# Kernel optimization log

Hardware: AMD Instinct MI355X
Metric: run time of the kernel (lower is better)

The kernel has to match this reference:

```python
import jax, jax.numpy as jnp
import numpy as np

CH_IN, CH_OUT, CH, NLAYERS = 40, 9, 64, 10
CH_CLOSE = 2 * CH
KSZ = 9  # stencil hard-coded to 9 in init_weights
H = 0.1


def conv1(X, Ker):
    # F.conv1d(X, Ker, padding=(k-1)//2); Ker: (Cout, Cin, k)
    pad = (Ker.shape[-1] - 1) // 2
    return jax.lax.conv_general_dilated(X, Ker, (1,), [(pad, pad)],
                                        dimension_numbers=('NCH', 'OIH', 'NCH'))


def conv1T(X, Ker):
    # F.conv_transpose1d(X, Ker, padding=(k-1)//2) with stride 1 ==
    # conv1d with swapped in/out channels and flipped taps, padding k-1-(k-1)//2
    k = Ker.shape[-1]
    pad = k - 1 - (k - 1) // 2
    Kt = jnp.flip(jnp.swapaxes(Ker, 0, 1), -1)
    return jax.lax.conv_general_dilated(X, Kt, (1,), [(pad, pad)],
                                        dimension_numbers=('NCH', 'OIH', 'NCH'))


def mean_masked(X, mask, axis, keepdims=False):
    return jnp.sum(X * mask, axis=axis, keepdims=keepdims) / jnp.sum(mask, axis=axis, keepdims=keepdims)


def tr2dist(Y):
    # pairwise distances of columns of Y (B,C,N) -> (B,N,N), per Pfold tr2DistSmall
    k = Y.shape[1]
    Z = Y - jnp.mean(Y, axis=2, keepdims=True)
    n2 = jnp.sum(Z * Z, axis=1)  # (B,N)
    D = n2[:, :, None] + n2[:, None, :] - 2.0 * jnp.einsum('bcn,bcm->bnm', Z, Z)
    D = 3.0 * D / k
    Dr = jnp.maximum(D, 0.0)
    safe = jnp.where(Dr > 0, Dr, 1.0)  # grad-safe sqrt
    return jnp.where(Dr > 0, jnp.sqrt(safe), 0.0)


def get_graph_lap(X, mask, sigma):
    # X: (B,C,N), mask: (B,1,N)
    mm = jnp.einsum('bci,bcj->bij', mask, mask)  # (B,N,N) pair mask
    msum = jnp.sum(mask, axis=2, keepdims=True)
    Xc = X - (jnp.sum(X * mask, axis=2, keepdims=True) / msum) * mask
    Xc = Xc / jnp.sqrt(jnp.sum(Xc * Xc, axis=2, keepdims=True) / msum + 1e-4)
    N = X.shape[2]
    pos = 0.5 * jnp.linspace(0.0, 1.0, N)[None, None, :] * mask  # (B,1,N)
    Xa = jnp.concatenate([Xc, pos], axis=1)
    W = tr2dist(Xa) * mm
    W = jnp.exp(-W / sigma * 10.0) * mm
    Wsum = jnp.sum(W, axis=1)  # (B,N)
    D = Wsum[:, :, None] * jnp.eye(N, dtype=W.dtype)  # diag(Wsum)
    L = D - W
    return 0.5 * (L + jnp.swapaxes(L, 1, 2)), W


def double_sym(Z, Wi, Bi, L, mask):
    A0 = conv1(Z + Bi[0], Wi[0]) * mask
    A0 = (A0 - mean_masked(A0, mask, 2, True)) * mask
    A0 = A0 / jnp.sqrt(jnp.sum(A0 * A0, axis=1, keepdims=True) + 1e-3)
    A1 = (conv1(Z + Bi[1], Wi[1]) @ L) * mask
    A1 = (A1 - mean_masked(A1, mask, 2, True)) * mask
    A1 = A1 / jnp.sqrt(jnp.sum(A1 * A1, axis=1, keepdims=True) + 1e-3)
    A0 = jax.nn.relu(A0)
    A1 = jax.nn.relu(A1)
    A0 = conv1T(A0, Wi[0]) * mask
    A1 = (conv1T(A1, Wi[1]) @ L) * mask
    return A0 + A1


def hypernet_forward(Z, mask, Kopen, Kclose, W, Bias):
    mask = mask[:, None, :]  # (B,1,N)
    Z = jnp.einsum('ci,bin->bcn', Kopen, Z) * mask
    L, _ = get_graph_lap(Z, mask, 10.0)
    for i in range(W.shape[0]):
        if i % 10 == 0:
            L, _ = get_graph_lap(Z, mask, 10.0)
        Z = Z - H * double_sym(Z, W[i], Bias[i], L, mask)
    Z = jnp.einsum('oc,bcn->bon', Kclose, Z) * mask
    dists = jnp.stack([tr2dist(Z[:, 3 * i:3 * i + 3, :]) for i in range(Z.shape[1] // 3)], axis=1)
    return dists, Z  # dists: (B, chan_out//3, N, N)


def setup_inputs() -> dict:
    key = jax.random.key(0)
    ks = jax.random.split(key, 5)
    B, N = 8, 1024
    Z = jax.random.normal(ks[0], (B, CH_IN, N), dtype=jnp.float32)
    mask = jnp.ones((B, N), dtype=jnp.float32)
    so = float(CH) / CH_IN
    Kopen = jax.random.uniform(ks[1], (CH, CH_IN), minval=-so, maxval=so, dtype=jnp.float32)
    sc = float(CH_OUT) / CH
    Kclose = jax.random.uniform(ks[2], (CH_OUT, CH), minval=-sc, maxval=sc, dtype=jnp.float32)
    W = jax.random.uniform(ks[3], (NLAYERS, 2, CH_CLOSE, CH, KSZ), minval=-0.1, maxval=0.1, dtype=jnp.float32)
    Bias = jax.random.uniform(ks[4], (NLAYERS, 2, CH, 1), dtype=jnp.float32) * 0.001
    return {"Z": Z, "mask": mask, "Kopen": Kopen, "Kclose": Kclose, "W": W, "Bias": Bias}


def reference(Z, mask, Kopen, Kclose, W, Bias):
    return hypernet_forward(Z, mask, Kopen, Kclose, W, Bias)
```

## Files before the change

kernel.cpp:

```cpp
#include <hip/hip_runtime.h>
#include <cstddef>

#define BB 8
#define NN 1024
#define CIN 40
#define CH 64
#define CC 128
#define COUT 9
#define KS 9
#define NL 10
#define HSTEP 0.1f
#define SKC 2
#define SKH 4

typedef __attribute__((ext_vector_type(8))) short bf16x8;
typedef __attribute__((ext_vector_type(4))) float f32x4;

__device__ __forceinline__ unsigned short f2bf(float f) {
    union { float f; unsigned u; } v;
    v.f = f;
    unsigned u = v.u;
    u += 0x7FFFu + ((u >> 16) & 1u);
    return (unsigned short)(u >> 16);
}
__device__ __forceinline__ float bf2f(unsigned short h) {
    union { unsigned u; float f; } v;
    v.u = ((unsigned)h) << 16;
    return v.f;
}

__device__ __forceinline__ size_t pk_addr(int lb, int row, int col, int R, int KDv) {
    int chunk = ((lb * (R / 32) + (row >> 5)) * (KDv / 32) + (col >> 5)) * 2 + ((row >> 4) & 1);
    int lane = ((col >> 3) & 3) * 16 + (row & 15);
    return ((size_t)chunk * 64 + lane) * 8 + (col & 7);
}

__device__ __forceinline__ float blockSum(float v, float* red) {
    int tid = threadIdx.x;
    red[tid] = v;
    __syncthreads();
    for (int s = 128; s > 0; s >>= 1) {
        if (tid < s) red[tid] += red[tid + s];
        __syncthreads();
    }
    float r = red[0];
    __syncthreads();
    return r;
}

__global__ __launch_bounds__(256) void k_zero(float* __restrict__ p, int n) {
    int i = blockIdx.x * 256 + threadIdx.x;
    if (i < n) p[i] = 0.f;
}

__global__ __launch_bounds__(256) void k_prep_wbf(const float* __restrict__ Win,
                                                  unsigned short* __restrict__ PKc_h,
                                                  unsigned short* __restrict__ PKc_l,
                                                  unsigned short* __restrict__ PKt_h,
                                                  unsigned short* __restrict__ PKt_l) {
    int idx = blockIdx.x * 256 + threadIdx.x;
    const int total = NL * 2 * CC * CH * KS;
    if (idx >= total) return;
    int k = idx % KS;
    int t = idx / KS;
    int i = t % CH;  t /= CH;
    int o = t % CC;  t /= CC;
    int lb = t;
    float v = Win[idx];
    unsigned short h = f2bf(v);
    unsigned short l = f2bf(v - bf2f(h));
    size_t ac = pk_addr(lb, o, k * 64 + i, CC, 576);
    size_t at = pk_addr(lb, i, (8 - k) * 128 + o, CH, 1152);
    PKc_h[ac] = h;
    PKc_l[ac] = l;
    PKt_h[at] = h;
    PKt_l[at] = l;
}

__global__ __launch_bounds__(256) void k_prep_bks(const float* __restrict__ Win,
                                                  const float* __restrict__ Bias,
                                                  float* __restrict__ bks) {
    int idx = blockIdx.x * 256 + threadIdx.x;
    const int total = NL * 2 * CC * KS;
    if (idx >= total) return;
    int k = idx % KS;
    int t = idx / KS;
    int o = t % CC;
    int lb = t / CC;
    float s = 0.f;
    for (int i = 0; i < CH; ++i)
        s += Win[(((size_t)lb * CC + o) * CH + i) * KS + k] * Bias[lb * CH + i];
    bks[idx] = s;
}

__global__ __launch_bounds__(256) void k_open(const float* __restrict__ Zin,
                                              const float* __restrict__ mask,
                                              const float* __restrict__ Kop,
                                              float* __restrict__ Zcur) {
    int n = blockIdx.x * 256 + threadIdx.x;
    int c = blockIdx.y, b = blockIdx.z;
    float acc = 0.f;
    for (int i = 0; i < CIN; ++i)
        acc += Kop[c * CIN + i] * Zin[((size_t)b * CIN + i) * NN + n];
    Zcur[((size_t)b * CH + c) * NN + n] = acc * mask[b * NN + n];
}

__global__ __launch_bounds__(256) void k_za(const float* __restrict__ Zcur,
                                            const float* __restrict__ mask,
                                            float* __restrict__ Za) {
    __shared__ float red[256];
    int c = blockIdx.x;
    int b = blockIdx.y;
    int tid = threadIdx.x;
    const float* m = mask + b * NN;
    float x[4], mv[4];
    if (c < CH) {
        const float* src = Zcur + ((size_t)b * CH + c) * NN;
#pragma unroll
        for (int j = 0; j < 4; ++j) { int n = tid * 4 + j; x[j] = src[n]; mv[j] = m[n]; }
    } else {
#pragma unroll
        for (int j = 0; j < 4; ++j) { int n = tid * 4 + j; mv[j] = m[n]; x[j] = 0.5f * ((float)n / 1023.f) * mv[j]; }
    }
    float sm = 0.f, sxm = 0.f;
#pragma unroll
    for (int j = 0; j < 4; ++j) { sm += mv[j]; sxm += x[j] * mv[j]; }
    float msum = blockSum(sm, red);
    float xm = blockSum(sxm, red);
    if (c < CH) {
        float mean = xm / msum;
        float ss = 0.f;
#pragma unroll
        for (int j = 0; j < 4; ++j) { x[j] -= mean * mv[j]; ss += x[j] * x[j]; }
        ss = blockSum(ss, red);
        float sc = rsqrtf(ss / msum + 1e-4f);
#pragma unroll
        for (int j = 0; j < 4; ++j) x[j] *= sc;
    }
    float ps = 0.f;
#pragma unroll
    for (int j = 0; j < 4; ++j) ps += x[j];
    float pm = blockSum(ps, red) / (float)NN;
    float* dst = Za + ((size_t)b * 65 + c) * NN;
#pragma unroll
    for (int j = 0; j < 4; ++j) dst[tid * 4 + j] = x[j] - pm;
}

__global__ __launch_bounds__(256) void k_n2g(const float* __restrict__ Za, float* __restrict__ n2g) {
    int n = blockIdx.x * 256 + threadIdx.x;
    int b = blockIdx.y;
    float s = 0.f;
    for (int c = 0; c < 65; ++c) { float v = Za[((size_t)b * 65 + c) * NN + n]; s += v * v; }
    n2g[b * NN + n] = s;
}

__global__ __launch_bounds__(256) void k_gramW(const float* __restrict__ Za,
                                               const float* __restrict__ n2g,
                                               const float* __restrict__ mask,
                                               unsigned short* __restrict__ Wpk,
                                               float* __restrict__ Wsum) {
    __shared__ float As[65][64];
    __shared__ float Bs2[65][64];
    __shared__ unsigned short wt[64][72];
    __shared__ float csred[16][64];
    int i0 = blockIdx.x * 64, j0 = blockIdx.y * 64, b = blockIdx.z;
    int tid = threadIdx.x;
    for (int e = tid; e < 65 * 64; e += 256) {
        int c = e >> 6, t = e & 63;
        const float* src = Za + ((size_t)b * 65 + c) * NN;
        As[c][t] = src[i0 + t];
        Bs2[c][t] = src[j0 + t];
    }
    __syncthreads();
    int tx = tid & 15, ty = tid >> 4;
    float acc[4][4] = {};
    for (int c = 0; c < 65; ++c) {
        float a[4];
#pragma unroll
        for (int q = 0; q < 4; ++q) a[q] = As[c][ty * 4 + q];
        float bv[4];
        *reinterpret_cast<float4*>(bv) = *reinterpret_cast<const float4*>(&Bs2[c][tx * 4]);
#pragma unroll
        for (int q = 0; q < 4; ++q)
#pragma unroll
            for (int r = 0; r < 4; ++r) acc[q][r] += a[q] * bv[r];
    }
    const float* m = mask + b * NN;
    float csacc[4] = {0.f, 0.f, 0.f, 0.f};
    for (int q = 0; q < 4; ++q) {
        int i = i0 + ty * 4 + q;
        float n2i = n2g[b * NN + i], mi = m[i];
#pragma unroll
        for (int r = 0; r < 4; ++r) {
            int j = j0 + tx * 4 + r;
            float D = n2i + n2g[b * NN + j] - 2.f * acc[q][r];
            D *= (3.f / 65.f);
            D = fmaxf(D, 0.f);
            float dist = (D > 0.f) ? sqrtf(D) : 0.f;
            float mmv = mi * m[j];
            float res = expf(-dist * mmv) * mmv;
            wt[ty * 4 + q][tx * 4 + r] = f2bf(res);
            csacc[r] += res;
        }
    }
#pragma unroll
    for (int r = 0; r < 4; ++r) csred[ty][tx * 4 + r] = csacc[r];
    __syncthreads();
    for (int s = 8; s > 0; s >>= 1) {
        if (ty < s) {
#pragma unroll
            for (int r = 0; r < 4; ++r) csred[ty][tx * 4 + r] += csred[ty + s][tx * 4 + r];
        }
        __syncthreads();
    }
    if (ty == 0) {
#pragma unroll
        for (int r = 0; r < 4; ++r)
            atomicAdd(&Wsum[b * NN + j0 + tx * 4 + r], csred[0][tx * 4 + r]);
    }
    for (int e = tid; e < 512; e += 256) {
        int li = e >> 3, ljb = (e & 7) * 8;
        int row = i0 + li, col = j0 + ljb;
        int chunk = ((b * 32 + (row >> 5)) * 32 + (col >> 5)) * 2 + ((row >> 4) & 1);
        int lane2 = ((col >> 3) & 3) * 16 + (row & 15);
        unsigned short* dp = Wpk + ((size_t)chunk * 64 + lane2) * 8;
        *reinterpret_cast<ushort4*>(dp) = *reinterpret_cast<ushort4*>(&wt[li][ljb]);
        *reinterpret_cast<ushort4*>(dp + 4) = *reinterpret_cast<ushort4*>(&wt[li][ljb + 4]);
    }
}

__global__ __launch_bounds__(256) void k_conv1_mfma(const float* __restrict__ Zcur,
                                                    const unsigned short* __restrict__ Wh,
                                                    const unsigned short* __restrict__ Wl,
                                                    const float* __restrict__ bksl,
                                                    const float* __restrict__ mask,
                                                    float* __restrict__ C0,
                                                    float* __restrict__ C1,
                                                    unsigned short* __restrict__ C1pk) {
    __shared__ __align__(16) unsigned short xh[80][64];
    __shared__ __align__(16) unsigned short xl[80][64];
    int n0 = blockIdx.x * 64;
    int y = blockIdx.y;
    int b = blockIdx.z;
    int br = y >> 1, half = y & 1;
    int tid = threadIdx.x;
    const float* Xb = Zcur + (size_t)b * CH * NN;

    for (int e = tid; e < 64 * 20; e += 256) {
        int i = e / 20, t = e - i * 20;
        int gn = n0 + t * 4 - 4;
        float4 v = make_float4(0.f, 0.f, 0.f, 0.f);
        if (gn >= 0 && gn + 3 < NN) v = *reinterpret_cast<const float4*>(&Xb[(size_t)i * NN + gn]);
        float vv[4] = {v.x, v.y, v.z, v.w};
#pragma unroll
        for (int j = 0; j < 4; ++j) {
            int row = t * 4 + j;
            int col = i ^ ((row & 7) << 3);
            unsigned short h = f2bf(vv[j]);
            xh[row][col] = h;
            xl[row][col] = f2bf(vv[j] - bf2f(h));
        }
    }
    __syncthreads();

    int wid = tid >> 6, lane = tid & 63;
    int wo = (wid >> 1) * 32, wn = (wid & 1) * 32;
    int r = lane & 15, g = lane >> 4;
    int r32 = half * 2 + (wid >> 1);
    size_t brOff = (size_t)br * (CC / 32) * (576 / 32) * 1024;

    f32x4 acc[2][2] = {};
#pragma unroll 3
    for (int q = 0; q < 18; ++q) {
        int k = q >> 1, s = q & 1;
        size_t widx = brOff + ((size_t)(r32 * 18 + q)) * 1024 + lane * 8;
        bf16x8 ah[2], al[2];
        ah[0] = *reinterpret_cast<const bf16x8*>(&Wh[widx]);
        ah[1] = *reinterpret_cast<const bf16x8*>(&Wh[widx + 512]);
        al[0] = *reinterpret_cast<const bf16x8*>(&Wl[widx]);
        al[1] = *reinterpret_cast<const bf16x8*>(&Wl[widx + 512]);
        bf16x8 bh[2], bl[2];
#pragma unroll
        for (int fn = 0; fn < 2; ++fn) {
            int row = wn + fn * 16 + r + k;
            int chs = (s * 32 + g * 8) ^ ((row & 7) << 3);
            bh[fn] = *reinterpret_cast<const bf16x8*>(&xh[row][chs]);
            bl[fn] = *reinterpret_cast<const bf16x8*>(&xl[row][chs]);
        }
#pragma unroll
        for (int fc = 0; fc < 2; ++fc)
#pragma unroll
            for (int fn = 0; fn < 2; ++fn) {
                acc[fc][fn] = __builtin_amdgcn_mfma_f32_16x16x32_bf16(ah[fc], bh[fn], acc[fc][fn], 0, 0, 0);
                acc[fc][fn] = __builtin_amdgcn_mfma_f32_16x16x32_bf16(al[fc], bh[fn], acc[fc][fn], 0, 0, 0);
                acc[fc][fn] = __builtin_amdgcn_mfma_f32_16x16x32_bf16(ah[fc], bl[fn], acc[fc][fn], 0, 0, 0);
            }
    }

    const float* mkB = mask + b * NN;
    float* Outp = (br ? C1 : C0) + ((size_t)b * CC + half * 64) * NN;
    const float* bo_base = bksl + (br * CC + half * 64) * KS;
#pragma unroll
    for (int fc = 0; fc < 2; ++fc) {
#pragma unroll
        for (int fn = 0; fn < 2; ++fn) {
            int n = n0 + wn + fn * 16 + r;
#pragma unroll
            for (int rr = 0; rr < 4; ++rr) {
                int oo = wo + fc * 16 + 4 * g + rr;
                float v = acc[fc][fn][rr];
                const float* bo = bo_base + oo * KS;
                float bias = 0.f;
#pragma unroll
                for (int k = 0; k < KS; ++k) {
                    int nn2 = n + k - 4;
                    if (nn2 >= 0 && nn2 < NN) bias += bo[k];
                }
                v += bias;
                if (br == 0) v *= mkB[n];
                Outp[(size_t)oo * NN + n] = v;
                if (br == 1) {
                    int cg = half * 64 + oo;
                    int chunk = ((b * 4 + (cg >> 5)) * 32 + (n >> 5)) * 2 + ((cg >> 4) & 1);
                    int lane2 = ((n >> 3) & 3) * 16 + (cg & 15);
                    C1pk[((size_t)chunk * 64 + lane2) * 8 + (n & 7)] = f2bf(v);
                }
            }
        }
    }
}

__global__ __launch_bounds__(256) void k_convT_mfma(const float* __restrict__ C0,
                                                    const float* __restrict__ A1,
                                                    const unsigned short* __restrict__ Wh,
                                                    const unsigned short* __restrict__ Wl,
                                                    const float* __restrict__ mask,
                                                    const float* __restrict__ meanA,
                                                    const float* __restrict__ invA,
                                                    float* __restrict__ T0,
                                                    float* __restrict__ T1p,
                                                    unsigned short* __restrict__ T1pk) {
    __shared__ __align__(16) unsigned short xh[48][128];
    __shared__ __align__(16) unsigned short xl[48][128];
    __shared__ float red2[2][32][33];
    int n0 = blockIdx.x * 32;
    int br = blockIdx.y;
    int b = blockIdx.z;
    int tid = threadIdx.x;
    const float* Xb = (br ? A1 : C0) + (size_t)b * CC * NN;
    const float* meB = meanA + ((size_t)br * BB + b) * CC;
    const float* ivB = invA + ((size_t)br * BB + b) * NN;
    const float* mkB = mask + b * NN;

    for (int e = tid; e < 128 * 12; e += 256) {
        int i = e / 12, t = e - i * 12;
        int gn = n0 + t * 4 - 4;
        float4 v = make_float4(0.f, 0.f, 0.f, 0.f);
        if (gn >= 0 && gn + 3 < NN) {
            v = *reinterpret_cast<const float4*>(&Xb[(size_t)i * NN + gn]);
            float me = meB[i];
            float4 iv = *reinterpret_cast<const float4*>(&ivB[gn]);
            float4 mk = *reinterpret_cast<const float4*>(&mkB[gn]);
            v.x = fmaxf((v.x - me) * mk.x * iv.x, 0.f);
            v.y = fmaxf((v.y - me) * mk.y * iv.y, 0.f);
            v.z = fmaxf((v.z - me) * mk.z * iv.z, 0.f);
            v.w = fmaxf((v.w - me) * mk.w * iv.w, 0.f);
        }
        float vv[4] = {v.x, v.y, v.z, v.w};
#pragma unroll
        for (int j = 0; j < 4; ++j) {
            int row = t * 4 + j;
            int col = i ^ ((row & 7) << 3);
            unsigned short h = f2bf(vv[j]);
            xh[row][col] = h;
            xl[row][col] = f2bf(vv[j] - bf2f(h));
        }
    }
    __syncthreads();

    int wid = tid >> 6, lane = tid & 63;
    int i32 = wid & 1, kh = wid >> 1;
    int r = lane & 15, g = lane >> 4;
    size_t brW = (size_t)br * (CH / 32) * (1152 / 32) * 1024;

    f32x4 acc[2][2] = {};
#pragma unroll 3
    for (int t = 0; t < 18; ++t) {
        int k = t >> 1, s = kh * 2 + (t & 1);
        int q32 = k * 4 + s;
        size_t widx = brW + ((size_t)(i32 * 36 + q32)) * 1024 + lane * 8;
        bf16x8 ah[2], al[2];
        ah[0] = *reinterpret_cast<const bf16x8*>(&Wh[widx]);
        ah[1] = *reinterpret_cast<const bf16x8*>(&Wh[widx + 512]);
        al[0] = *reinterpret_cast<const bf16x8*>(&Wl[widx]);
        al[1] = *reinterpret_cast<const bf16x8*>(&Wl[widx + 512]);
        bf16x8 bh[2], bl[2];
#pragma unroll
        for (int fn = 0; fn < 2; ++fn) {
            int row = fn * 16 + r + k;
            int chs = (s * 32 + g * 8) ^ ((row & 7) << 3);
            bh[fn] = *reinterpret_cast<const bf16x8*>(&xh[row][chs]);
            bl[fn] = *reinterpret_cast<const bf16x8*>(&xl[row][chs]);
        }
#pragma unroll
        for (int fc = 0; fc < 2; ++fc)
#pragma unroll
            for (int fn = 0; fn < 2; ++fn) {
                acc[fc][fn] = __builtin_amdgcn_mfma_f32_16x16x32_bf16(ah[fc], bh[fn], acc[fc][fn], 0, 0, 0);
                acc[fc][fn] = __builtin_amdgcn_mfma_f32_16x16x32_bf16(al[fc], bh[fn], acc[fc][fn], 0, 0, 0);
                acc[fc][fn] = __builtin_amdgcn_mfma_f32_16x16x32_bf16(ah[fc], bl[fn], acc[fc][fn], 0, 0, 0);
            }
    }

    if (kh == 1) {
#pragma unroll
        for (int fc = 0; fc < 2; ++fc)
#pragma unroll
            for (int fn = 0; fn < 2; ++fn)
#pragma unroll
                for (int rr = 0; rr < 4; ++rr)
                    red2[i32][fc * 16 + 4 * g + rr][fn * 16 + r] = acc[fc][fn][rr];
    }
    __syncthreads();
    if (kh == 0) {
        float* Outp = (br ? T1p : T0) + (size_t)b * CH * NN;
#pragma unroll
        for (int fc = 0; fc < 2; ++fc)
#pragma unroll
            for (int fn = 0; fn < 2; ++fn) {
                int n = n0 + fn * 16 + r;
#pragma unroll
                for (int rr = 0; rr < 4; ++rr) {
                    int irow = fc * 16 + 4 * g + rr;
                    float v = acc[fc][fn][rr] + red2[i32][irow][fn * 16 + r];
                    Outp[(size_t)(i32 * 32 + irow) * NN + n] = v;
                    if (br == 1) {
                        int cg = i32 * 32 + irow;
                        int chunk = ((b * 2 + (cg >> 5)) * 32 + (n >> 5)) * 2 + ((cg >> 4) & 1);
                        int lane2 = ((n >> 3) & 3) * 16 + (cg & 15);
                        T1pk[((size_t)chunk * 64 + lane2) * 8 + (n & 7)] = f2bf(v);
                    }
                }
            }
    }
}

template <int SKN>
__global__ __launch_bounds__(256) void k_matL_mfma(const unsigned short* __restrict__ Xpk,
                                                   const unsigned short* __restrict__ Wpk,
                                                   float* __restrict__ Part, int rows) {
    int cb = rows >> 6;
    int sk = blockIdx.y;
    int b = blockIdx.z / cb;
    int c0 = (blockIdx.z % cb) * 64;
    int tid = threadIdx.x;
    int wid = tid >> 6, lane = tid & 63;
    int wc = (wid >> 1) * 32;
    int r = lane & 15, g = lane >> 4;
    int rowsT = rows >> 5;
    int ct = (c0 >> 5) + (wid >> 1);
    int nt32 = blockIdx.x * 2 + (wid & 1);
    const unsigned short* Xb = Xpk + ((size_t)(b * rowsT + ct)) * 32768 + (size_t)lane * 8;
    const unsigned short* Wb = Wpk + ((size_t)(b * 32 + nt32)) * 32768 + (size_t)lane * 8;

    f32x4 acc[2][2] = {};
    int ms_beg = sk * (32 / SKN);
#pragma unroll 4
    for (int ms = ms_beg; ms < ms_beg + 32 / SKN; ++ms) {
        bf16x8 a0 = *reinterpret_cast<const bf16x8*>(&Xb[(size_t)ms * 1024]);
        bf16x8 a1 = *reinterpret_cast<const bf16x8*>(&Xb[(size_t)ms * 1024 + 512]);
        bf16x8 w0 = *reinterpret_cast<const bf16x8*>(&Wb[(size_t)ms * 1024]);
        bf16x8 w1 = *reinterpret_cast<const bf16x8*>(&Wb[(size_t)ms * 1024 + 512]);
        acc[0][0] = __builtin_amdgcn_mfma_f32_16x16x32_bf16(a0, w0, acc[0][0], 0, 0, 0);
        acc[0][1] = __builtin_amdgcn_mfma_f32_16x16x32_bf16(a0, w1, acc[0][1], 0, 0, 0);
        acc[1][0] = __builtin_amdgcn_mfma_f32_16x16x32_bf16(a1, w0, acc[1][0], 0, 0, 0);
        acc[1][1] = __builtin_amdgcn_mfma_f32_16x16x32_bf16(a1, w1, acc[1][1], 0, 0, 0);
    }
    int n0 = blockIdx.x * 64;
    int wn = (wid & 1) * 32;
#pragma unroll
    for (int fc = 0; fc < 2; ++fc)
#pragma unroll
        for (int fn = 0; fn < 2; ++fn) {
            int ncol = n0 + wn + fn * 16 + r;
#pragma unroll
            for (int rr = 0; rr < 4; ++rr) {
                int crow = c0 + wc + fc * 16 + 4 * g + rr;
                Part[(((size_t)b * SKN + sk) * rows + crow) * NN + ncol] = acc[fc][fn][rr];
            }
        }
}

template <int SKN, int MODE>
__global__ __launch_bounds__(256) void k_matL_fin(const float* __restrict__ X,
                                                  const float* __restrict__ Part,
                                                  const float* __restrict__ Wsum,
                                                  const float* __restrict__ mask,
                                                  const float* __restrict__ T0,
                                                  float* __restrict__ Out,
                                                  float* __restrict__ meanA, int rows) {
    __shared__ float red[256];
    int c = blockIdx.x, b = blockIdx.y;
    int n = threadIdx.x * 4;
    float4 s = make_float4(0.f, 0.f, 0.f, 0.f);
#pragma unroll
    for (int sk = 0; sk < SKN; ++sk) {
        float4 p = *reinterpret_cast<const float4*>(
            &Part[(((size_t)b * SKN + sk) * rows + c) * NN + n]);
        s.x += p.x; s.y += p.y; s.z += p.z; s.w += p.w;
    }
    float4 xv = *reinterpret_cast<const float4*>(&X[((size_t)b * rows + c) * NN + n]);
    float4 wv = *reinterpret_cast<const float4*>(&Wsum[b * NN + n]);
    float4 mv = *reinterpret_cast<const float4*>(&mask[b * NN + n]);
    float y0 = xv.x * wv.x - s.x, y1 = xv.y * wv.y - s.y;
    float y2 = xv.z * wv.z - s.z, y3 = xv.w * wv.w - s.w;
    if (MODE == 0) {
        float4 res = make_float4(y0 * mv.x, y1 * mv.y, y2 * mv.z, y3 * mv.w);
        *reinterpret_cast<float4*>(&Out[((size_t)b * rows + c) * NN + n]) = res;
        float rs = res.x * mv.x + res.y * mv.y + res.z * mv.z + res.w * mv.w;
        float ms = mv.x + mv.y + mv.z + mv.w;
        rs = blockSum(rs, red);
        ms = blockSum(ms, red);
        if (threadIdx.x == 0) meanA[((size_t)BB + b) * CC + c] = rs / ms;
    } else {
        float4 t0 = *reinterpret_cast<const float4*>(&T0[((size_t)b * rows + c) * NN + n]);
        float4 o = *reinterpret_cast<const float4*>(&Out[((size_t)b * rows + c) * NN + n]);
        float4 res = make_float4(o.x - HSTEP * mv.x * (t0.x + y0),
                                 o.y - HSTEP * mv.y * (t0.y + y1),
                                 o.z - HSTEP * mv.z * (t0.z + y2),
                                 o.w - HSTEP * mv.w * (t0.w + y3));
        *reinterpret_cast<float4*>(&Out[((size_t)b * rows + c) * NN + n]) = res;
    }
}

__global__ __launch_bounds__(256) void k_rowmean(const float* __restrict__ X0,
                                                 const float* __restrict__ mask,
                                                 float* __restrict__ meanA) {
    __shared__ float red[256];
    int c = blockIdx.x, b = blockIdx.y, tid = threadIdx.x;
    const float* src = X0 + ((size_t)b * CC + c) * NN;
    const float* m = mask + b * NN;
    float s = 0.f, sm = 0.f;
    for (int n = tid; n < NN; n += 256) { float mv = m[n]; s += src[n] * mv; sm += mv; }
    float ts = blockSum(s, red);
    float tm = blockSum(sm, red);
    if (tid == 0) meanA[(size_t)b * CC + c] = ts / tm;
}

__global__ __launch_bounds__(256) void k_colnorm_inv(const float* __restrict__ X0,
                                                     const float* __restrict__ X1,
                                                     const float* __restrict__ mask,
                                                     const float* __restrict__ meanA,
                                                     float* __restrict__ invA) {
    __shared__ float red[8][32];
    int tid = threadIdx.x;
    int nl = tid & 31, cg = tid >> 5;
    int n = blockIdx.x * 32 + nl;
    int b = blockIdx.y, z = blockIdx.z;
    const float* X = (z ? X1 : X0) + (size_t)b * CC * NN;
    const float* me = meanA + ((size_t)z * BB + b) * CC;
    float mv = mask[b * NN + n];
    float ss = 0.f;
#pragma unroll
    for (int cc = 0; cc < 16; ++cc) {
        int c = cg * 16 + cc;
        float v = (X[(size_t)c * NN + n] - me[c]) * mv;
        ss += v * v;
    }
    red[cg][nl] = ss;
    __syncthreads();
    if (cg < 4) red[cg][nl] += red[cg + 4][nl];
    __syncthreads();
    if (cg < 2) red[cg][nl] += red[cg + 2][nl];
    __syncthreads();
    if (cg < 1) red[0][nl] += red[1][nl];
    __syncthreads();
    if (cg == 0) invA[((size_t)z * BB + b) * NN + n] = rsqrtf(red[0][nl] + 0.001f);
}

__global__ __launch_bounds__(256) void k_close(const float* __restrict__ Zcur,
                                               const float* __restrict__ Kcl,
                                               const float* __restrict__ mask,
                                               float* __restrict__ Zout) {
    __shared__ float red[4][64][COUT];
    int tid = threadIdx.x;
    int nl = tid & 63, cg = tid >> 6;
    int n = blockIdx.x * 64 + nl;
    int b = blockIdx.y;
    float acc[COUT] = {};
#pragma unroll
    for (int cc = 0; cc < 16; ++cc) {
        int c = cg * 16 + cc;
        float zv = Zcur[((size_t)b * CH + c) * NN + n];
#pragma unroll
        for (int o = 0; o < COUT; ++o) acc[o] += Kcl[o * CH + c] * zv;
    }
#pragma unroll
    for (int o = 0; o < COUT; ++o) red[cg][nl][o] = acc[o];
    __syncthreads();
    if (cg == 0) {
        float mv = mask[b * NN + n];
#pragma unroll
        for (int o = 0; o < COUT; ++o) {
            float s = red[0][nl][o] + red[1][nl][o] + red[2][nl][o] + red[3][nl][o];
            Zout[((size_t)b * COUT + o) * NN + n] = s * mv;
        }
    }
}

__global__ __launch_bounds__(256) void k_center3(const float* __restrict__ Zout, float* __restrict__ Zc3) {
    __shared__ float red[256];
    int c = blockIdx.x, b = blockIdx.y, tid = threadIdx.x;
    const float* src = Zout + ((size_t)b * COUT + c) * NN;
    float s = 0.f;
    for (int n = tid; n < NN; n += 256) s += src[n];
    float mean = blockSum(s, red) / (float)NN;
    float* dst = Zc3 + ((size_t)b * COUT + c) * NN;
    for (int n = tid; n < NN; n += 256) dst[n] = src[n] - mean;
}

__global__ __launch_bounds__(256) void k_n23(const float* __restrict__ Zc3, float* __restrict__ n23) {
    int n = blockIdx.x * 256 + threadIdx.x;
    int g = blockIdx.y, b = blockIdx.z;
    float s = 0.f;
#pragma unroll
    for (int c = 0; c < 3; ++c) { float v = Zc3[((size_t)b * COUT + g * 3 + c) * NN + n]; s += v * v; }
    n23[((size_t)b * 3 + g) * NN + n] = s;
}

__global__ __launch_bounds__(256) void k_dist(const float* __restrict__ Zc3,
                                              const float* __restrict__ n23,
                                              float* __restrict__ dout) {
    __shared__ float Ai[3][64], Aj[3][64], ni[64], nj[64];
    int bg = blockIdx.z;
    int b = bg / 3, g = bg - 3 * b;
    int i0 = blockIdx.x * 64, j0 = blockIdx.y * 64;
    int tid = threadIdx.x;
    if (tid < 64) ni[tid] = n23[((size_t)b * 3 + g) * NN + i0 + tid];
    else if (tid < 128) { int t = tid - 64; nj[t] = n23[((size_t)b * 3 + g) * NN + j0 + t]; }
    for (int e = tid; e < 192; e += 256) {
        int c = e / 64, t = e - c * 64;
        Ai[c][t] = Zc3[((size_t)b * COUT + g * 3 + c) * NN + i0 + t];
    }
    for (int e = tid; e < 192; e += 256) {
        int c = e / 64, t = e - c * 64;
        Aj[c][t] = Zc3[((size_t)b * COUT + g * 3 + c) * NN + j0 + t];
    }
    __syncthreads();
    int tx = tid & 15, ty = tid >> 4;
    for (int q = 0; q < 4; ++q) {
        int i = ty * 4 + q;
        float a0 = Ai[0][i], a1 = Ai[1][i], a2 = Ai[2][i], n2i = ni[i];
        float res[4];
#pragma unroll
        for (int r = 0; r < 4; ++r) {
            int j = tx * 4 + r;
            float D = n2i + nj[j] - 2.f * (a0 * Aj[0][j] + a1 * Aj[1][j] + a2 * Aj[2][j]);
            D = fmaxf(D, 0.f);
            res[r] = (D > 0.f) ? sqrtf(D) : 0.f;
        }
        *reinterpret_cast<float4*>(&dout[(((size_t)b * 3 + g) * NN + i0 + i) * NN + j0 + tx * 4]) =
            *reinterpret_cast<float4*>(res);
    }
}

extern "C" void kernel_launch(void* const* d_in, const int* in_sizes, int n_in,
                              void* d_out, int out_size, void* d_ws, size_t ws_size,
                              hipStream_t stream) {
    (void)in_sizes; (void)n_in; (void)out_size; (void)ws_size;
    const float* Zin  = (const float*)d_in[0];
    const float* mask = (const float*)d_in[1];
    const float* Kop  = (const float*)d_in[2];
    const float* Kcl  = (const float*)d_in[3];
    const float* Win  = (const float*)d_in[4];
    const float* Bias = (const float*)d_in[5];
    float* out = (float*)d_out;
    float* ws = (float*)d_ws;

    size_t off = 0;
    float* Zcur = ws + off;  off += (size_t)BB * CH * NN;
    float* C0   = ws + off;  off += (size_t)BB * CC * NN;
    float* C1   = ws + off;  off += (size_t)BB * CC * NN;
    float* A1   = ws + off;  off += (size_t)BB * CC * NN;
    float* T0   = ws + off;  off += (size_t)BB * CH * NN;
    float* T1p  = ws + off;  off += (size_t)BB * CH * NN;
    float* Za   = ws + off;  off += (size_t)BB * 65 * NN;
    float* n2g  = ws + off;  off += (size_t)BB * NN;
    float* Wsum = ws + off;  off += (size_t)BB * NN;
    float* meanA= ws + off;  off += (size_t)2 * BB * CC;
    float* bks  = ws + off;  off += (size_t)NL * 2 * CC * KS;
    float* Zc3  = ws + off;  off += (size_t)BB * COUT * NN;
    float* n23  = ws + off;  off += (size_t)BB * 3 * NN;
    float* invA = ws + off;  off += (size_t)2 * BB * NN;

    float* Part = out;
    unsigned short* Wpk2  = (unsigned short*)(out + (size_t)4194304);
    unsigned short* C1pk  = (unsigned short*)(out + (size_t)8388608);
    unsigned short* T1pk  = (unsigned short*)(out + (size_t)8912896);
    unsigned short* PKc_h = (unsigned short*)(out + (size_t)14680064);
    unsigned short* PKc_l = (unsigned short*)(out + (size_t)15417344);
    unsigned short* PKt_h = (unsigned short*)(out + (size_t)16154624);
    unsigned short* PKt_l = (unsigned short*)(out + (size_t)16891904);

    const int wtot = NL * 2 * CC * CH * KS;
    k_prep_wbf<<<dim3((wtot + 255) / 256), 256, 0, stream>>>(Win, PKc_h, PKc_l, PKt_h, PKt_l);
    k_prep_bks<<<dim3((NL * 2 * CC * KS + 255) / 256), 256, 0, stream>>>(Win, Bias, bks);
    k_zero<<<dim3(BB * NN / 256), 256, 0, stream>>>(Wsum, BB * NN);
    k_open<<<dim3(NN / 256, CH, BB), 256, 0, stream>>>(Zin, mask, Kop, Zcur);
    k_za<<<dim3(65, BB), 256, 0, stream>>>(Zcur, mask, Za);
    k_n2g<<<dim3(NN / 256, BB), 256, 0, stream>>>(Za, n2g);
    k_gramW<<<dim3(16, 16, BB), 256, 0, stream>>>(Za, n2g, mask, Wpk2, Wsum);

    for (int l = 0; l < NL; ++l) {
        const unsigned short* PKc_h_l = PKc_h + (size_t)l * 2 * CC * 576;
        const unsigned short* PKc_l_l = PKc_l + (size_t)l * 2 * CC * 576;
        const unsigned short* PKt_h_l = PKt_h + (size_t)l * 2 * CH * 1152;
        const unsigned short* PKt_l_l = PKt_l + (size_t)l * 2 * CH * 1152;
        const float* bksl = bks + (size_t)l * 2 * CC * KS;

        k_conv1_mfma<<<dim3(NN / 64, 4, BB), 256, 0, stream>>>(
            Zcur, PKc_h_l, PKc_l_l, bksl, mask, C0, C1, C1pk);
        k_matL_mfma<SKC><<<dim3(NN / 64, SKC, BB * (CC / 64)), 256, 0, stream>>>(C1pk, Wpk2, Part, CC);
        k_matL_fin<SKC, 0><<<dim3(CC, BB), 256, 0, stream>>>(
            C1, Part, Wsum, mask, nullptr, A1, meanA, CC);
        k_rowmean<<<dim3(CC, BB), 256, 0, stream>>>(C0, mask, meanA);
        k_colnorm_inv<<<dim3(NN / 32, BB, 2), 256, 0, stream>>>(C0, A1, mask, meanA, invA);
        k_convT_mfma<<<dim3(NN / 32, 2, BB), 256, 0, stream>>>(
            C0, A1, PKt_h_l, PKt_l_l, mask, meanA, invA, T0, T1p, T1pk);
        k_matL_mfma<SKH><<<dim3(NN / 64, SKH, BB * (CH / 64)), 256, 0, stream>>>(T1pk, Wpk2, Part, CH);
        k_matL_fin<SKH, 1><<<dim3(CH, BB), 256, 0, stream>>>(
            T1p, Part, Wsum, mask, T0, Zcur, nullptr, CH);
    }

    float* Zout = out + (size_t)BB * 3 * NN * NN;
    k_close<<<dim3(NN / 64, BB), 256, 0, stream>>>(Zcur, Kcl, mask, Zout);
    k_center3<<<dim3(COUT, BB), 256, 0, stream>>>(Zout, Zc3);
    k_n23<<<dim3(NN / 256, 3, BB), 256, 0, stream>>>(Zc3, n23);
    k_dist<<<dim3(16, 16, 3 * BB), 256, 0, stream>>>(Zc3, n23, out);
}
```

Measured before the change: 869.1 us.

## Fuse norm and mean helper kernels into gram, convT, matL_fin and dist kernels

Removes the separate k_n2g, k_n23, k_rowmean and k_colnorm_inv launches. Squared norms are now computed in shared memory inside k_gramW and k_dist. The C0 row mean moves into k_matL_fin, and the per-column inverse norm moves into k_convT_mfma by staging the centered tile in a float shared buffer. This cuts 2 launches per layer plus 2 one-time launches and their global round trips. In exchange, convT recomputes column norms across the halo columns of each block, uses more shared memory (possible occupancy loss) and adds extra syncs. The gram kernel also pads its shared arrays.

```diff
diff --git a/kernel.cpp b/kernel.cpp
--- a/kernel.cpp
+++ b/kernel.cpp
@@ -146,23 +146,15 @@
     for (int j = 0; j < 4; ++j) dst[tid * 4 + j] = x[j] - pm;
 }
 
-__global__ __launch_bounds__(256) void k_n2g(const float* __restrict__ Za, float* __restrict__ n2g) {
-    int n = blockIdx.x * 256 + threadIdx.x;
-    int b = blockIdx.y;
-    float s = 0.f;
-    for (int c = 0; c < 65; ++c) { float v = Za[((size_t)b * 65 + c) * NN + n]; s += v * v; }
-    n2g[b * NN + n] = s;
-}
-
 __global__ __launch_bounds__(256) void k_gramW(const float* __restrict__ Za,
-                                               const float* __restrict__ n2g,
                                                const float* __restrict__ mask,
                                                unsigned short* __restrict__ Wpk,
                                                float* __restrict__ Wsum) {
-    __shared__ float As[65][64];
-    __shared__ float Bs2[65][64];
+    __shared__ float As[65][68];
+    __shared__ float Bs2[65][68];
     __shared__ unsigned short wt[64][72];
     __shared__ float csred[16][64];
+    __shared__ float n2is[64], n2js[64];
     int i0 = blockIdx.x * 64, j0 = blockIdx.y * 64, b = blockIdx.z;
     int tid = threadIdx.x;
     for (int e = tid; e < 65 * 64; e += 256) {
@@ -172,6 +164,17 @@
         Bs2[c][t] = src[j0 + t];
     }
     __syncthreads();
+    if (tid < 64) {
+        float s = 0.f;
+        for (int c = 0; c < 65; ++c) { float v = As[c][tid]; s += v * v; }
+        n2is[tid] = s;
+    } else if (tid < 128) {
+        int t = tid - 64;
+        float s = 0.f;
+        for (int c = 0; c < 65; ++c) { float v = Bs2[c][t]; s += v * v; }
+        n2js[t] = s;
+    }
+    __syncthreads();
     int tx = tid & 15, ty = tid >> 4;
     float acc[4][4] = {};
     for (int c = 0; c < 65; ++c) {
@@ -189,11 +192,11 @@
     float csacc[4] = {0.f, 0.f, 0.f, 0.f};
     for (int q = 0; q < 4; ++q) {
         int i = i0 + ty * 4 + q;
-        float n2i = n2g[b * NN + i], mi = m[i];
+        float n2i = n2is[ty * 4 + q], mi = m[i];
 #pragma unroll
         for (int r = 0; r < 4; ++r) {
             int j = j0 + tx * 4 + r;
-            float D = n2i + n2g[b * NN + j] - 2.f * acc[q][r];
+            float D = n2i + n2js[tx * 4 + r] - 2.f * acc[q][r];
             D *= (3.f / 65.f);
             D = fmaxf(D, 0.f);
             float dist = (D > 0.f) ? sqrtf(D) : 0.f;
@@ -336,20 +339,21 @@
                                                     const unsigned short* __restrict__ Wl,
                                                     const float* __restrict__ mask,
                                                     const float* __restrict__ meanA,
-                                                    const float* __restrict__ invA,
                                                     float* __restrict__ T0,
                                                     float* __restrict__ T1p,
                                                     unsigned short* __restrict__ T1pk) {
+    __shared__ float fs[48][132];
     __shared__ __align__(16) unsigned short xh[48][128];
     __shared__ __align__(16) unsigned short xl[48][128];
     __shared__ float red2[2][32][33];
+    __shared__ float ps[48][4];
+    __shared__ float invc[48];
     int n0 = blockIdx.x * 32;
     int br = blockIdx.y;
     int b = blockIdx.z;
     int tid = threadIdx.x;
     const float* Xb = (br ? A1 : C0) + (size_t)b * CC * NN;
     const float* meB = meanA + ((size_t)br * BB + b) * CC;
-    const float* ivB = invA + ((size_t)br * BB + b) * NN;
     const float* mkB = mask + b * NN;
 
     for (int e = tid; e < 128 * 12; e += 256) {
@@ -359,21 +363,38 @@
         if (gn >= 0 && gn + 3 < NN) {
             v = *reinterpret_cast<const float4*>(&Xb[(size_t)i * NN + gn]);
             float me = meB[i];
-            float4 iv = *reinterpret_cast<const float4*>(&ivB[gn]);
             float4 mk = *reinterpret_cast<const float4*>(&mkB[gn]);
-            v.x = fmaxf((v.x - me) * mk.x * iv.x, 0.f);
-            v.y = fmaxf((v.y - me) * mk.y * iv.y, 0.f);
-            v.z = fmaxf((v.z - me) * mk.z * iv.z, 0.f);
-            v.w = fmaxf((v.w - me) * mk.w * iv.w, 0.f);
-        }
-        float vv[4] = {v.x, v.y, v.z, v.w};
+            v.x = (v.x - me) * mk.x;
+            v.y = (v.y - me) * mk.y;
+            v.z = (v.z - me) * mk.z;
+            v.w = (v.w - me) * mk.w;
+        }
+        fs[t * 4 + 0][i] = v.x;
+        fs[t * 4 + 1][i] = v.y;
+        fs[t * 4 + 2][i] = v.z;
+        fs[t * 4 + 3][i] = v.w;
+    }
+    __syncthreads();
+    if (tid < 192) {
+        int row = tid % 48, seg = tid / 48;
+        float ss = 0.f;
+#pragma unroll
+        for (int i = 0; i < 32; ++i) { float v = fs[row][seg * 32 + i]; ss += v * v; }
+        ps[row][seg] = ss;
+    }
+    __syncthreads();
+    if (tid < 48) invc[tid] = rsqrtf(ps[tid][0] + ps[tid][1] + ps[tid][2] + ps[tid][3] + 0.001f);
+    __syncthreads();
+    for (int e = tid; e < 128 * 12; e += 256) {
+        int i = e / 12, t = e - i * 12;
 #pragma unroll
         for (int j = 0; j < 4; ++j) {
             int row = t * 4 + j;
+            float v = fmaxf(fs[row][i] * invc[row], 0.f);
             int col = i ^ ((row & 7) << 3);
-            unsigned short h = f2bf(vv[j]);
+            unsigned short h = f2bf(v);
             xh[row][col] = h;
-            xl[row][col] = f2bf(vv[j] - bf2f(h));
+            xl[row][col] = f2bf(v - bf2f(h));
         }
     }
     __syncthreads();
@@ -498,7 +519,8 @@
                                                   const float* __restrict__ mask,
                                                   const float* __restrict__ T0,
                                                   float* __restrict__ Out,
-                                                  float* __restrict__ meanA, int rows) {
+                                                  float* __restrict__ meanA, int rows,
+                                                  const float* __restrict__ C0p) {
     __shared__ float red[256];
     int c = blockIdx.x, b = blockIdx.y;
     int n = threadIdx.x * 4;
@@ -517,11 +539,17 @@
     if (MODE == 0) {
         float4 res = make_float4(y0 * mv.x, y1 * mv.y, y2 * mv.z, y3 * mv.w);
         *reinterpret_cast<float4*>(&Out[((size_t)b * rows + c) * NN + n]) = res;
+        float4 c0v = *reinterpret_cast<const float4*>(&C0p[((size_t)b * rows + c) * NN + n]);
         float rs = res.x * mv.x + res.y * mv.y + res.z * mv.z + res.w * mv.w;
+        float cs = c0v.x * mv.x + c0v.y * mv.y + c0v.z * mv.z + c0v.w * mv.w;
         float ms = mv.x + mv.y + mv.z + mv.w;
         rs = blockSum(rs, red);
+        cs = blockSum(cs, red);
         ms = blockSum(ms, red);
-        if (threadIdx.x == 0) meanA[((size_t)BB + b) * CC + c] = rs / ms;
+        if (threadIdx.x == 0) {
+            meanA[(size_t)b * CC + c] = cs / ms;
+            meanA[((size_t)BB + b) * CC + c] = rs / ms;
+        }
     } else {
         float4 t0 = *reinterpret_cast<const float4*>(&T0[((size_t)b * rows + c) * NN + n]);
         float4 o = *reinterpret_cast<const float4*>(&Out[((size_t)b * rows + c) * NN + n]);
@@ -531,51 +559,6 @@
                                  o.w - HSTEP * mv.w * (t0.w + y3));
         *reinterpret_cast<float4*>(&Out[((size_t)b * rows + c) * NN + n]) = res;
     }
-}
-
-__global__ __launch_bounds__(256) void k_rowmean(const float* __restrict__ X0,
-                                                 const float* __restrict__ mask,
-                                                 float* __restrict__ meanA) {
-    __shared__ float red[256];
-    int c = blockIdx.x, b = blockIdx.y, tid = threadIdx.x;
-    const float* src = X0 + ((size_t)b * CC + c) * NN;
-    const float* m = mask + b * NN;
-    float s = 0.f, sm = 0.f;
-    for (int n = tid; n < NN; n += 256) { float mv = m[n]; s += src[n] * mv; sm += mv; }
-    float ts = blockSum(s, red);
-    float tm = blockSum(sm, red);
-    if (tid == 0) meanA[(size_t)b * CC + c] = ts / tm;
-}
-
-__global__ __launch_bounds__(256) void k_colnorm_inv(const float* __restrict__ X0,
-                                                     const float* __restrict__ X1,
-                                                     const float* __restrict__ mask,
-                                                     const float* __restrict__ meanA,
-                                                     float* __restrict__ invA) {
-    __shared__ float red[8][32];
-    int tid = threadIdx.x;
-    int nl = tid & 31, cg = tid >> 5;
-    int n = blockIdx.x * 32 + nl;
-    int b = blockIdx.y, z = blockIdx.z;
-    const float* X = (z ? X1 : X0) + (size_t)b * CC * NN;
-    const float* me = meanA + ((size_t)z * BB + b) * CC;
-    float mv = mask[b * NN + n];
-    float ss = 0.f;
-#pragma unroll
-    for (int cc = 0; cc < 16; ++cc) {
-        int c = cg * 16 + cc;
-        float v = (X[(size_t)c * NN + n] - me[c]) * mv;
-        ss += v * v;
-    }
-    red[cg][nl] = ss;
-    __syncthreads();
-    if (cg < 4) red[cg][nl] += red[cg + 4][nl];
-    __syncthreads();
-    if (cg < 2) red[cg][nl] += red[cg + 2][nl];
-    __syncthreads();
-    if (cg < 1) red[0][nl] += red[1][nl];
-    __syncthreads();
-    if (cg == 0) invA[((size_t)z * BB + b) * NN + n] = rsqrtf(red[0][nl] + 0.001f);
 }
 
 __global__ __launch_bounds__(256) void k_close(const float* __restrict__ Zcur,
@@ -619,25 +602,13 @@
     for (int n = tid; n < NN; n += 256) dst[n] = src[n] - mean;
 }
 
-__global__ __launch_bounds__(256) void k_n23(const float* __restrict__ Zc3, float* __restrict__ n23) {
-    int n = blockIdx.x * 256 + threadIdx.x;
-    int g = blockIdx.y, b = blockIdx.z;
-    float s = 0.f;
-#pragma unroll
-    for (int c = 0; c < 3; ++c) { float v = Zc3[((size_t)b * COUT + g * 3 + c) * NN + n]; s += v * v; }
-    n23[((size_t)b * 3 + g) * NN + n] = s;
-}
-
 __global__ __launch_bounds__(256) void k_dist(const float* __restrict__ Zc3,
-                                              const float* __restrict__ n23,
                                               float* __restrict__ dout) {
     __shared__ float Ai[3][64], Aj[3][64], ni[64], nj[64];
     int bg = blockIdx.z;
     int b = bg / 3, g = bg - 3 * b;
     int i0 = blockIdx.x * 64, j0 = blockIdx.y * 64;
     int tid = threadIdx.x;
-    if (tid < 64) ni[tid] = n23[((size_t)b * 3 + g) * NN + i0 + tid];
-    else if (tid < 128) { int t = tid - 64; nj[t] = n23[((size_t)b * 3 + g) * NN + j0 + t]; }
     for (int e = tid; e < 192; e += 256) {
         int c = e / 64, t = e - c * 64;
         Ai[c][t] = Zc3[((size_t)b * COUT + g * 3 + c) * NN + i0 + t];
@@ -645,6 +616,13 @@
     for (int e = tid; e < 192; e += 256) {
         int c = e / 64, t = e - c * 64;
         Aj[c][t] = Zc3[((size_t)b * COUT + g * 3 + c) * NN + j0 + t];
+    }
+    __syncthreads();
+    if (tid < 64) {
+        ni[tid] = Ai[0][tid] * Ai[0][tid] + Ai[1][tid] * Ai[1][tid] + Ai[2][tid] * Ai[2][tid];
+    } else if (tid < 128) {
+        int t = tid - 64;
+        nj[t] = Aj[0][t] * Aj[0][t] + Aj[1][t] * Aj[1][t] + Aj[2][t] * Aj[2][t];
     }
     __syncthreads();
     int tx = tid & 15, ty = tid >> 4;
@@ -685,13 +663,10 @@
     float* T0   = ws + off;  off += (size_t)BB * CH * NN;
     float* T1p  = ws + off;  off += (size_t)BB * CH * NN;
     float* Za   = ws + off;  off += (size_t)BB * 65 * NN;
-    float* n2g  = ws + off;  off += (size_t)BB * NN;
     float* Wsum = ws + off;  off += (size_t)BB * NN;
     float* meanA= ws + off;  off += (size_t)2 * BB * CC;
     float* bks  = ws + off;  off += (size_t)NL * 2 * CC * KS;
     float* Zc3  = ws + off;  off += (size_t)BB * COUT * NN;
-    float* n23  = ws + off;  off += (size_t)BB * 3 * NN;
-    float* invA = ws + off;  off += (size_t)2 * BB * NN;
 
     float* Part = out;
     unsigned short* Wpk2  = (unsigned short*)(out + (size_t)4194304);
@@ -708,8 +683,7 @@
     k_zero<<<dim3(BB * NN / 256), 256, 0, stream>>>(Wsum, BB * NN);
     k_open<<<dim3(NN / 256, CH, BB), 256, 0, stream>>>(Zin, mask, Kop, Zcur);
     k_za<<<dim3(65, BB), 256, 0, stream>>>(Zcur, mask, Za);
-    k_n2g<<<dim3(NN / 256, BB), 256, 0, stream>>>(Za, n2g);
-    k_gramW<<<dim3(16, 16, BB), 256, 0, stream>>>(Za, n2g, mask, Wpk2, Wsum);
+    k_gramW<<<dim3(16, 16, BB), 256, 0, stream>>>(Za, mask, Wpk2, Wsum);
 
     for (int l = 0; l < NL; ++l) {
         const unsigned short* PKc_h_l = PKc_h + (size_t)l * 2 * CC * 576;
@@ -722,19 +696,16 @@
             Zcur, PKc_h_l, PKc_l_l, bksl, mask, C0, C1, C1pk);
         k_matL_mfma<SKC><<<dim3(NN / 64, SKC, BB * (CC / 64)), 256, 0, stream>>>(C1pk, Wpk2, Part, CC);
         k_matL_fin<SKC, 0><<<dim3(CC, BB), 256, 0, stream>>>(
-            C1, Part, Wsum, mask, nullptr, A1, meanA, CC);
-        k_rowmean<<<dim3(CC, BB), 256, 0, stream>>>(C0, mask, meanA);
-        k_colnorm_inv<<<dim3(NN / 32, BB, 2), 256, 0, stream>>>(C0, A1, mask, meanA, invA);
+            C1, Part, Wsum, mask, nullptr, A1, meanA, CC, C0);
         k_convT_mfma<<<dim3(NN / 32, 2, BB), 256, 0, stream>>>(
-            C0, A1, PKt_h_l, PKt_l_l, mask, meanA, invA, T0, T1p, T1pk);
+            C0, A1, PKt_h_l, PKt_l_l, mask, meanA, T0, T1p, T1pk);
         k_matL_mfma<SKH><<<dim3(NN / 64, SKH, BB * (CH / 64)), 256, 0, stream>>>(T1pk, Wpk2, Part, CH);
         k_matL_fin<SKH, 1><<<dim3(CH, BB), 256, 0, stream>>>(
-            T1p, Part, Wsum, mask, T0, Zcur, nullptr, CH);
+            T1p, Part, Wsum, mask, T0, Zcur, nullptr, CH, nullptr);
     }
 
     float* Zout = out + (size_t)BB * 3 * NN * NN;
     k_close<<<dim3(NN / 64, BB), 256, 0, stream>>>(Zcur, Kcl, mask, Zout);
     k_center3<<<dim3(COUT, BB), 256, 0, stream>>>(Zout, Zc3);
-    k_n23<<<dim3(NN / 256, 3, BB), 256, 0, stream>>>(Zc3, n23);
-    k_dist<<<dim3(16, 16, 3 * BB), 256, 0, stream>>>(Zc3, n23, out);
-}
+    k_dist<<<dim3(16, 16, 3 * BB), 256, 0, stream>>>(Zc3, out);
+}
```

Measured after the change: 817.7 us. 5.9% less time.
